# Kernel optimization log

Measured on AMD Instinct MI355X. Metric: run time of the kernel, lower is better.

The kernel has to match this reference:

```python
import jax, jax.numpy as jnp
import numpy as np

B, T, N, KH, DH, KS = 8, 64, 128, 8, 64, 3  # batch, num_step, num_vertex, heads, head_dim, kernel
D = KH * DH
EPS = 1e-5


def setup_inputs() -> dict:
    key = jax.random.key(0)
    ks = jax.random.split(key, 8)
    s = 0.02
    return {
        "X": jax.random.normal(ks[0], (B, T, N, D), dtype=jnp.float32),
        # causal conv Q/K: torch Conv2d weight [out, in, 1, ks]
        "Wq": jax.random.normal(ks[1], (D, D, 1, KS), dtype=jnp.float32) * s,
        "bq": jnp.zeros((D,), jnp.float32),
        "gq": jnp.ones((D,), jnp.float32),
        "betaq": jnp.zeros((D,), jnp.float32),
        "mq": jnp.zeros((D,), jnp.float32),
        "vq": jnp.ones((D,), jnp.float32),
        "Wk": jax.random.normal(ks[2], (D, D, 1, KS), dtype=jnp.float32) * s,
        "bk": jnp.zeros((D,), jnp.float32),
        "gk": jnp.ones((D,), jnp.float32),
        "betak": jnp.zeros((D,), jnp.float32),
        "mk": jnp.zeros((D,), jnp.float32),
        "vk": jnp.ones((D,), jnp.float32),
        # torch Linear weights [out, in]
        "Wv": jax.random.normal(ks[3], (D, D), dtype=jnp.float32) * s,
        "bv": jnp.zeros((D,), jnp.float32),
        "Wo": jax.random.normal(ks[4], (D, D), dtype=jnp.float32) * s,
        "bo": jnp.zeros((D,), jnp.float32),
    }


def _causal_conv(x, W, b):
    # x: [B, D, N, T]; left-pad time by ks-1 == torch pad-both-then-slice[:-pad]
    pad = W.shape[-1] - 1
    y = jax.lax.conv_general_dilated(
        x, W, window_strides=(1, 1), padding=((0, 0), (pad, 0)),
        dimension_numbers=("NCHW", "OIHW", "NCHW"))
    return y + b[None, :, None, None]


def _bn(x, g, beta, m, v):
    # eval-mode BatchNorm2d over channel dim 1
    inv = jax.lax.rsqrt(v + EPS)
    return (x - m[None, :, None, None]) * (g * inv)[None, :, None, None] + beta[None, :, None, None]


def reference(X, Wq, bq, gq, betaq, mq, vq, Wk, bk, gk, betak, mk, vk, Wv, bv, Wo, bo):
    b, t, n, dm = X.shape
    X_ = X.transpose(0, 3, 2, 1)                       # [B, D, N, T]
    q = _bn(_causal_conv(X_, Wq, bq), gq, betaq, mq, vq).transpose(0, 3, 2, 1)  # [B,T,N,D]
    k = _bn(_causal_conv(X_, Wk, bk), gk, betak, mk, vk).transpose(0, 3, 2, 1)  # [B,T,N,D]
    v = jnp.einsum("btnd,ed->btne", X, Wv) + bv        # FC_v
    # split heads (equivalent to split/cat along batch in the original)
    qh = q.reshape(b, t, n, KH, DH)
    kh = k.reshape(b, t, n, KH, DH)
    vh = v.reshape(b, t, n, KH, DH)
    scores = jnp.einsum("bqnhd,bpnhd->bnhqp", qh, kh) * (DH ** -0.5)  # [B,N,H,T,T]
    attn = jax.nn.softmax(scores, axis=-1)
    out = jnp.einsum("bnhqp,bpnhd->bqnhd", attn, vh).reshape(b, t, n, dm)
    out = jnp.einsum("btnd,ed->btne", out, Wo) + bo    # FC
    return out  # [B, T, N, D]
```

## Files before the change

kernel.cpp:

```cpp
#include <hip/hip_runtime.h>

typedef unsigned short u16;
typedef u16    u16x4  __attribute__((ext_vector_type(4)));
typedef u16    u16x8  __attribute__((ext_vector_type(8)));
typedef __bf16 bf16x8 __attribute__((ext_vector_type(8)));
typedef float  f32x4  __attribute__((ext_vector_type(4)));
typedef float  f32x16 __attribute__((ext_vector_type(16)));

#define DEV static __device__ __forceinline__

DEV float bf2f(u16 h) {
    union { unsigned int u; float f; } c; c.u = ((unsigned int)h) << 16; return c.f;
}
DEV u16 f2bf(float f) {
    union { float f; unsigned int u; } c; c.f = f;
    unsigned int u = c.u + 0x7FFFu + ((c.u >> 16) & 1u);
    return (u16)(u >> 16);
}
DEV bf16x8 ld8(const u16* p) {
    return __builtin_bit_cast(bf16x8, *(const u16x8*)p);
}
DEV void gload_lds16(const u16* g, u16* l) {
    __builtin_amdgcn_global_load_lds((__attribute__((address_space(1))) void*)g,
                                     (__attribute__((address_space(3))) void*)l,
                                     16, 0, 0);
}

__global__ __launch_bounds__(256) void f32_to_bf16(
    const float* __restrict__ src, u16* __restrict__ dst, int n)
{
    int i = (blockIdx.x * 256 + threadIdx.x) * 4;
    if (i < n) {
        f32x4 v = *(const f32x4*)(src + i);
        u16x4 o;
        o[0] = f2bf(v[0]); o[1] = f2bf(v[1]); o[2] = f2bf(v[2]); o[3] = f2bf(v[3]);
        *(u16x4*)(dst + i) = o;
    }
}

__global__ __launch_bounds__(256) void prep_weights(
    const float* __restrict__ Wq, const float* __restrict__ gq, const float* __restrict__ vq,
    const float* __restrict__ Wk, const float* __restrict__ gk, const float* __restrict__ vk,
    u16* __restrict__ Wqt, u16* __restrict__ Wkt)
{
    int idx = blockIdx.x * 256 + threadIdx.x;
    int mat = idx >= 786432;
    int rem = idx - mat * 786432;
    int tap = rem / 262144;
    int oi  = rem - tap * 262144;
    int o = oi >> 9, i = oi & 511;
    const float* W = mat ? Wk : Wq;
    const float* g = mat ? gk : gq;
    const float* v = mat ? vk : vq;
    float s = g[o] * rsqrtf(v[o] + 1e-5f) * (mat ? 1.0f : 0.125f);
    float w = W[(o * 512 + i) * 3 + tap] * s;
    (mat ? Wkt : Wqt)[(tap * 512 + o) * 512 + i] = f2bf(w);
}

__global__ __launch_bounds__(256) void prep_bias(
    const float* bq, const float* gq, const float* betaq, const float* mq, const float* vq,
    const float* bk, const float* gk, const float* betak, const float* mk, const float* vk,
    float* __restrict__ biasq, float* __restrict__ biask)
{
    int o = blockIdx.x * 256 + threadIdx.x;
    if (o < 512) {
        float sq = gq[o] * rsqrtf(vq[o] + 1e-5f);
        biasq[o] = ((bq[o] - mq[o]) * sq + betaq[o]) * 0.125f;
        float sk = gk[o] * rsqrtf(vk[o] + 1e-5f);
        biask[o] = (bk[o] - mk[o]) * sk + betak[o];
    }
}

__global__ __launch_bounds__(256) void qkv_gemm(
    const u16* __restrict__ Xb,
    const u16* __restrict__ Wqt, const u16* __restrict__ Wkt, const u16* __restrict__ Wv,
    const float* __restrict__ biasq, const float* __restrict__ biask, const float* __restrict__ bv,
    u16* __restrict__ Qa, u16* __restrict__ Ka, u16* __restrict__ Va, int b0)
{
    __shared__ __align__(16) u16 As[128 * 64];
    __shared__ __align__(16) u16 Bs[128 * 64];

    const int which = blockIdx.x >> 2;
    const int cb    = (blockIdx.x & 3) * 128;
    const int rt    = blockIdx.y;
    const int brel  = rt >> 6;
    const int b     = b0 + brel;
    const int t     = rt & 63;

    const int tid  = threadIdx.x;
    const int wave = tid >> 6;
    const int lane = tid & 63;
    const int wm   = (wave & 1) * 64;
    const int wn   = (wave >> 1) * 64;
    const int l31  = lane & 31;
    const int q5   = lane >> 5;

    f32x16 acc[2][2];
#pragma unroll
    for (int mi = 0; mi < 2; mi++)
#pragma unroll
        for (int ni = 0; ni < 2; ni++)
#pragma unroll
            for (int e = 0; e < 16; e++) acc[mi][ni][e] = 0.f;

    const int ntaps = (which == 2) ? 1 : 3;
    const u16* Wbase0 = (which == 0) ? Wqt : (which == 1) ? Wkt : Wv;

    for (int tap = 0; tap < ntaps; ++tap) {
        int tsrc = (which == 2) ? t : (t + tap - 2);
        if (tsrc < 0) continue;
        const u16* Abase = Xb + ((size_t)(b * 64 + tsrc) * 128) * 512;
        const u16* Wbase = Wbase0 + (which == 2 ? 0 : (size_t)tap * 262144);

        for (int kk = 0; kk < 512; kk += 64) {
            __syncthreads();
#pragma unroll
            for (int i = 0; i < 4; ++i) {
                int p   = i * 256 + tid;
                int row = p >> 3;
                int sl  = (p & 7) ^ (row & 7);
                gload_lds16(Abase + (size_t)row * 512 + kk + sl * 8, As + p * 8);
                gload_lds16(Wbase + (size_t)(cb + row) * 512 + kk + sl * 8, Bs + p * 8);
            }
            __syncthreads();

#pragma unroll
            for (int half = 0; half < 2; ++half) {
                bf16x8 af[2][2], bf[2][2];
#pragma unroll
                for (int mi = 0; mi < 2; mi++) {
                    int r = wm + mi * 32 + l31;
#pragma unroll
                    for (int j = 0; j < 2; j++) {
                        int k2 = half * 2 + j;
                        af[mi][j] = ld8(As + ((r * 64 + k2 * 16 + q5 * 8) ^ ((r & 7) << 3)));
                    }
                }
#pragma unroll
                for (int ni = 0; ni < 2; ni++) {
                    int c = wn + ni * 32 + l31;
#pragma unroll
                    for (int j = 0; j < 2; j++) {
                        int k2 = half * 2 + j;
                        bf[ni][j] = ld8(Bs + ((c * 64 + k2 * 16 + q5 * 8) ^ ((c & 7) << 3)));
                    }
                }
#pragma unroll
                for (int j = 0; j < 2; j++)
#pragma unroll
                    for (int mi = 0; mi < 2; mi++)
#pragma unroll
                        for (int ni = 0; ni < 2; ni++)
                            acc[mi][ni] = __builtin_amdgcn_mfma_f32_32x32x16_bf16(
                                af[mi][j], bf[ni][j], acc[mi][ni], 0, 0, 0);
            }
        }
    }

    float biasv[2];
#pragma unroll
    for (int ni = 0; ni < 2; ni++) {
        int c = cb + wn + ni * 32 + l31;
        biasv[ni] = (which == 0) ? biasq[c] : (which == 1) ? biask[c] : bv[c];
    }
    u16* Outp = (which == 0) ? Qa : (which == 1) ? Ka : Va;
#pragma unroll
    for (int mi = 0; mi < 2; mi++) {
#pragma unroll
        for (int ni = 0; ni < 2; ni++) {
            int c = cb + wn + ni * 32 + l31;
            int h = c >> 6, dd = c & 63;
#pragma unroll
            for (int r = 0; r < 16; r++) {
                int n = wm + mi * 32 + (r & 3) + ((r >> 2) << 3) + (q5 << 2);
                float val = acc[mi][ni][r] + biasv[ni];
                size_t idx = ((((size_t)(brel * 128 + n)) * 8 + h) * 64 + t) * 64 + dd;
                Outp[idx] = f2bf(val);
            }
        }
    }
}

__global__ __launch_bounds__(256) void attn_kernel(
    const u16* __restrict__ Qa, const u16* __restrict__ Ka, const u16* __restrict__ Va,
    u16* __restrict__ AO)
{
    __shared__ __align__(16) u16 Qs[64 * 72];
    __shared__ __align__(16) u16 Ks[64 * 72];
    __shared__ __align__(16) u16 Vt[64 * 72];
    __shared__ __align__(16) u16 Ps[64 * 72];

    const int h = blockIdx.x, n = blockIdx.y, brel = blockIdx.z;
    const int tid = threadIdx.x, wave = tid >> 6, lane = tid & 63;
    const int l15 = lane & 15, q4 = lane >> 4;
    const size_t base = ((size_t)((brel * 128 + n) * 8 + h)) * 4096;

#pragma unroll
    for (int i = 0; i < 2; i++) {
        int chunk = i * 256 + tid;
        int row = chunk >> 3, kc = chunk & 7;
        u16x8 vq = *(const u16x8*)(Qa + base + chunk * 8);
        u16x8 vk = *(const u16x8*)(Ka + base + chunk * 8);
        u16x8 vv = *(const u16x8*)(Va + base + chunk * 8);
        *(u16x8*)(Qs + row * 72 + kc * 8) = vq;
        *(u16x8*)(Ks + row * 72 + kc * 8) = vk;
#pragma unroll
        for (int j = 0; j < 8; j++) Vt[(kc * 8 + j) * 72 + row] = vv[j];
    }
    __syncthreads();

    f32x4 s[4];
#pragma unroll
    for (int ni = 0; ni < 4; ni++) s[ni] = f32x4{0.f, 0.f, 0.f, 0.f};
    bf16x8 aq[2];
#pragma unroll
    for (int ks = 0; ks < 2; ks++)
        aq[ks] = ld8(Qs + (wave * 16 + l15) * 72 + ks * 32 + q4 * 8);
#pragma unroll
    for (int ni = 0; ni < 4; ni++) {
        int p = ni * 16 + l15;
#pragma unroll
        for (int ks = 0; ks < 2; ks++) {
            bf16x8 bk8 = ld8(Ks + p * 72 + ks * 32 + q4 * 8);
            s[ni] = __builtin_amdgcn_mfma_f32_16x16x32_bf16(aq[ks], bk8, s[ni], 0, 0, 0);
        }
    }

    float rmax[4], rsum[4], inv[4];
#pragma unroll
    for (int r = 0; r < 4; r++)
        rmax[r] = fmaxf(fmaxf(s[0][r], s[1][r]), fmaxf(s[2][r], s[3][r]));
#pragma unroll
    for (int m = 1; m < 16; m <<= 1)
#pragma unroll
        for (int r = 0; r < 4; r++)
            rmax[r] = fmaxf(rmax[r], __shfl_xor(rmax[r], m, 64));
    float e[4][4];
#pragma unroll
    for (int r = 0; r < 4; r++) rsum[r] = 0.f;
#pragma unroll
    for (int ni = 0; ni < 4; ni++)
#pragma unroll
        for (int r = 0; r < 4; r++) {
            e[ni][r] = __expf(s[ni][r] - rmax[r]);
            rsum[r] += e[ni][r];
        }
#pragma unroll
    for (int m = 1; m < 16; m <<= 1)
#pragma unroll
        for (int r = 0; r < 4; r++)
            rsum[r] += __shfl_xor(rsum[r], m, 64);
#pragma unroll
    for (int r = 0; r < 4; r++) inv[r] = 1.0f / rsum[r];

#pragma unroll
    for (int ni = 0; ni < 4; ni++)
#pragma unroll
        for (int r = 0; r < 4; r++)
            Ps[(wave * 16 + q4 * 4 + r) * 72 + ni * 16 + l15] = f2bf(e[ni][r]);
    __syncthreads();

    f32x4 o[4];
#pragma unroll
    for (int ni = 0; ni < 4; ni++) o[ni] = f32x4{0.f, 0.f, 0.f, 0.f};
    bf16x8 ap[2];
#pragma unroll
    for (int ks = 0; ks < 2; ks++)
        ap[ks] = ld8(Ps + (wave * 16 + l15) * 72 + ks * 32 + q4 * 8);
#pragma unroll
    for (int ni = 0; ni < 4; ni++) {
        int dd = ni * 16 + l15;
#pragma unroll
        for (int ks = 0; ks < 2; ks++) {
            bf16x8 bv8 = ld8(Vt + dd * 72 + ks * 32 + q4 * 8);
            o[ni] = __builtin_amdgcn_mfma_f32_16x16x32_bf16(ap[ks], bv8, o[ni], 0, 0, 0);
        }
    }

#pragma unroll
    for (int ni = 0; ni < 4; ni++) {
        int dd = ni * 16 + l15;
#pragma unroll
        for (int r = 0; r < 4; r++) {
            int tt = wave * 16 + q4 * 4 + r;
            AO[base + tt * 64 + dd] = f2bf(o[ni][r] * inv[r]);
        }
    }
}

__global__ __launch_bounds__(256) void proj_gemm(
    const u16* __restrict__ AO, const u16* __restrict__ Wo, const float* __restrict__ bo,
    float* __restrict__ Out, int b0)
{
    __shared__ __align__(16) u16 As[128 * 64];
    __shared__ __align__(16) u16 Bs[128 * 64];

    const int cb   = blockIdx.x * 128;
    const int rt   = blockIdx.y;
    const int brel = rt >> 6;
    const int b    = b0 + brel;
    const int t    = rt & 63;

    const int tid  = threadIdx.x;
    const int wave = tid >> 6;
    const int lane = tid & 63;
    const int wm   = (wave & 1) * 64;
    const int wn   = (wave >> 1) * 64;
    const int l31  = lane & 31;
    const int q5   = lane >> 5;

    f32x16 acc[2][2];
#pragma unroll
    for (int mi = 0; mi < 2; mi++)
#pragma unroll
        for (int ni = 0; ni < 2; ni++)
#pragma unroll
            for (int e = 0; e < 16; e++) acc[mi][ni][e] = 0.f;

    for (int kk = 0; kk < 512; kk += 64) {
        __syncthreads();
#pragma unroll
        for (int i = 0; i < 4; ++i) {
            int p   = i * 256 + tid;
            int row = p >> 3;
            int sl  = (p & 7) ^ (row & 7);
            int k   = kk + sl * 8;
            int hh  = k >> 6, d0 = k & 63;
            const u16* ga = AO + ((((size_t)(brel * 128 + row)) * 8 + hh) * 64 + t) * 64 + d0;
            gload_lds16(ga, As + p * 8);
            gload_lds16(Wo + (size_t)(cb + row) * 512 + k, Bs + p * 8);
        }
        __syncthreads();

#pragma unroll
        for (int half = 0; half < 2; ++half) {
            bf16x8 af[2][2], bf[2][2];
#pragma unroll
            for (int mi = 0; mi < 2; mi++) {
                int r = wm + mi * 32 + l31;
#pragma unroll
                for (int j = 0; j < 2; j++) {
                    int k2 = half * 2 + j;
                    af[mi][j] = ld8(As + ((r * 64 + k2 * 16 + q5 * 8) ^ ((r & 7) << 3)));
                }
            }
#pragma unroll
            for (int ni = 0; ni < 2; ni++) {
                int c = wn + ni * 32 + l31;
#pragma unroll
                for (int j = 0; j < 2; j++) {
                    int k2 = half * 2 + j;
                    bf[ni][j] = ld8(Bs + ((c * 64 + k2 * 16 + q5 * 8) ^ ((c & 7) << 3)));
                }
            }
#pragma unroll
            for (int j = 0; j < 2; j++)
#pragma unroll
                for (int mi = 0; mi < 2; mi++)
#pragma unroll
                    for (int ni = 0; ni < 2; ni++)
                        acc[mi][ni] = __builtin_amdgcn_mfma_f32_32x32x16_bf16(
                            af[mi][j], bf[ni][j], acc[mi][ni], 0, 0, 0);
        }
    }

#pragma unroll
    for (int mi = 0; mi < 2; mi++) {
#pragma unroll
        for (int ni = 0; ni < 2; ni++) {
            int c = cb + wn + ni * 32 + l31;
            float bias = bo[c];
#pragma unroll
            for (int r = 0; r < 16; r++) {
                int n = wm + mi * 32 + (r & 3) + ((r >> 2) << 3) + (q5 << 2);
                float val = acc[mi][ni][r] + bias;
                size_t idx = (((size_t)(b * 64 + t)) * 128 + n) * 512 + c;
                Out[idx] = val;
            }
        }
    }
}

extern "C" void kernel_launch(void* const* d_in, const int* in_sizes, int n_in,
                              void* d_out, int out_size, void* d_ws, size_t ws_size,
                              hipStream_t stream)
{
    const float* X     = (const float*)d_in[0];
    const float* Wq    = (const float*)d_in[1];
    const float* bq    = (const float*)d_in[2];
    const float* gq    = (const float*)d_in[3];
    const float* betaq = (const float*)d_in[4];
    const float* mq    = (const float*)d_in[5];
    const float* vq    = (const float*)d_in[6];
    const float* Wk    = (const float*)d_in[7];
    const float* bk    = (const float*)d_in[8];
    const float* gk    = (const float*)d_in[9];
    const float* betak = (const float*)d_in[10];
    const float* mk    = (const float*)d_in[11];
    const float* vk    = (const float*)d_in[12];
    const float* Wv    = (const float*)d_in[13];
    const float* bv    = (const float*)d_in[14];
    const float* Wo    = (const float*)d_in[15];
    const float* bo    = (const float*)d_in[16];
    float* outp = (float*)d_out;
    u16*   ws   = (u16*)d_ws;

    const size_t XTOT   = 33554432;
    const size_t XSLICE = 4194304;

    const bool big = ws_size >= (size_t)206000000;

    u16 *Xb, *Qa, *Ka, *Wqt;
    if (big) {
        Xb  = ws;
        Qa  = ws + XTOT;
        Ka  = Qa + XTOT;
        Wqt = Ka + XTOT;
    } else {
        Xb  = ws;
        Qa  = ws + XSLICE;
        Ka  = Qa + XSLICE;
        Wqt = Ka + XSLICE;
    }
    u16* Wkt = Wqt + 786432;
    u16* Wvb = Wkt + 786432;
    u16* Wob = Wvb + 262144;
    float* biasq = (float*)(Wob + 262144);
    float* biask = biasq + 512;

    hipLaunchKernelGGL(prep_weights, dim3(6144), dim3(256), 0, stream,
                       Wq, gq, vq, Wk, gk, vk, Wqt, Wkt);
    hipLaunchKernelGGL(prep_bias, dim3(2), dim3(256), 0, stream,
                       bq, gq, betaq, mq, vq, bk, gk, betak, mk, vk, biasq, biask);
    hipLaunchKernelGGL(f32_to_bf16, dim3(256), dim3(256), 0, stream, Wv, Wvb, 262144);
    hipLaunchKernelGGL(f32_to_bf16, dim3(256), dim3(256), 0, stream, Wo, Wob, 262144);

    if (big) {
        u16* Va = (u16*)d_out;
        hipLaunchKernelGGL(f32_to_bf16, dim3(32768), dim3(256), 0, stream,
                           X, Xb, (int)XTOT);
        hipLaunchKernelGGL(qkv_gemm, dim3(12, 512), dim3(256), 0, stream,
                           Xb, Wqt, Wkt, Wvb, biasq, biask, bv, Qa, Ka, Va, 0);
        hipLaunchKernelGGL(attn_kernel, dim3(8, 128, 8), dim3(256), 0, stream,
                           Qa, Ka, Va, Qa);
        hipLaunchKernelGGL(proj_gemm, dim3(4, 512), dim3(256), 0, stream,
                           Qa, Wob, bo, outp, 0);
    } else {
        for (int p = 0; p < 8; ++p) {
            u16* Va = (u16*)d_out + (size_t)p * 2 * XSLICE;
            hipLaunchKernelGGL(f32_to_bf16, dim3(4096), dim3(256), 0, stream,
                               X + (size_t)p * XSLICE, Xb, (int)XSLICE);
            hipLaunchKernelGGL(qkv_gemm, dim3(12, 64), dim3(256), 0, stream,
                               Xb - (size_t)p * XSLICE, Wqt, Wkt, Wvb,
                               biasq, biask, bv, Qa, Ka, Va, p);
            hipLaunchKernelGGL(attn_kernel, dim3(8, 128, 1), dim3(256), 0, stream,
                               Qa, Ka, Va, Qa);
            hipLaunchKernelGGL(proj_gemm, dim3(4, 64), dim3(256), 0, stream,
                               Qa, Wob, bo, outp, p);
        }
    }
}
```

Before: 634.1 us.

## Replace QKV GEMM with 256x256-tile double-buffered 8-wave kernel

Rewrites the fused Q/K/V projection as a 512-thread kernel. Each block computes a 256-row (two timesteps) by 256-column tile. The conv taps are folded into a single K=1536 loop using a tap-interleaved weight layout, and padded timesteps load from a zero buffer instead of taking a branch. LDS is double-buffered, with prefetch interleaved between MFMA phases, s_setprio, and block-index remapping for XCD locality. This is meant to cut LDS/global traffic per FLOP and hide load latency, at the cost of high register pressure (occupancy 1) and more barriers.

```diff
diff --git a/kernel.cpp b/kernel.cpp
--- a/kernel.cpp
+++ b/kernel.cpp
@@ -5,7 +5,6 @@
 typedef u16    u16x8  __attribute__((ext_vector_type(8)));
 typedef __bf16 bf16x8 __attribute__((ext_vector_type(8)));
 typedef float  f32x4  __attribute__((ext_vector_type(4)));
-typedef float  f32x16 __attribute__((ext_vector_type(16)));
 
 #define DEV static __device__ __forceinline__
 
@@ -25,6 +24,12 @@
                                      (__attribute__((address_space(3))) void*)l,
                                      16, 0, 0);
 }
+DEV void bar() {
+    asm volatile("" ::: "memory");
+    __builtin_amdgcn_s_barrier();
+    asm volatile("" ::: "memory");
+}
+#define VMCNT(n) asm volatile("s_waitcnt vmcnt(" #n ")" ::: "memory")
 
 __global__ __launch_bounds__(256) void f32_to_bf16(
     const float* __restrict__ src, u16* __restrict__ dst, int n)
@@ -54,13 +59,13 @@
     const float* v = mat ? vk : vq;
     float s = g[o] * rsqrtf(v[o] + 1e-5f) * (mat ? 1.0f : 0.125f);
     float w = W[(o * 512 + i) * 3 + tap] * s;
-    (mat ? Wkt : Wqt)[(tap * 512 + o) * 512 + i] = f2bf(w);
+    (mat ? Wkt : Wqt)[(o * 3 + tap) * 512 + i] = f2bf(w);
 }
 
 __global__ __launch_bounds__(256) void prep_bias(
     const float* bq, const float* gq, const float* betaq, const float* mq, const float* vq,
     const float* bk, const float* gk, const float* betak, const float* mk, const float* vk,
-    float* __restrict__ biasq, float* __restrict__ biask)
+    float* __restrict__ biasq, float* __restrict__ biask, u16* __restrict__ zb)
 {
     int o = blockIdx.x * 256 + threadIdx.x;
     if (o < 512) {
@@ -69,113 +74,166 @@
         float sk = gk[o] * rsqrtf(vk[o] + 1e-5f);
         biask[o] = (bk[o] - mk[o]) * sk + betak[o];
     }
-}
-
-__global__ __launch_bounds__(256) void qkv_gemm(
+    if (blockIdx.x == 0 && threadIdx.x < 64) zb[threadIdx.x] = 0;
+}
+
+__global__ __launch_bounds__(512, 1) void qkv8(
     const u16* __restrict__ Xb,
-    const u16* __restrict__ Wqt, const u16* __restrict__ Wkt, const u16* __restrict__ Wv,
+    const u16* __restrict__ Wq3, const u16* __restrict__ Wk3, const u16* __restrict__ Wv1,
     const float* __restrict__ biasq, const float* __restrict__ biask, const float* __restrict__ bv,
+    const u16* __restrict__ zbuf,
     u16* __restrict__ Qa, u16* __restrict__ Ka, u16* __restrict__ Va, int b0)
 {
-    __shared__ __align__(16) u16 As[128 * 64];
-    __shared__ __align__(16) u16 Bs[128 * 64];
-
-    const int which = blockIdx.x >> 2;
-    const int cb    = (blockIdx.x & 3) * 128;
-    const int rt    = blockIdx.y;
-    const int brel  = rt >> 6;
+    __shared__ __align__(16) u16 As[2 * 16384];
+    __shared__ __align__(16) u16 Bs[2 * 16384];
+
+    const int total = gridDim.x;
+    const int cpx   = total >> 3;
+    const int s     = blockIdx.x;
+    const int w     = (s & 7) * cpx + (s >> 3);
+    const int wc    = w % 6;
+    const int bt    = w / 6;
+    const int which = wc >> 1;
+    const int cb    = (wc & 1) * 256;
+    const int tpair = bt & 31;
+    const int brel  = bt >> 5;
     const int b     = b0 + brel;
-    const int t     = rt & 63;
 
     const int tid  = threadIdx.x;
     const int wave = tid >> 6;
     const int lane = tid & 63;
-    const int wm   = (wave & 1) * 64;
-    const int wn   = (wave >> 1) * 64;
-    const int l31  = lane & 31;
-    const int q5   = lane >> 5;
-
-    f32x16 acc[2][2];
-#pragma unroll
-    for (int mi = 0; mi < 2; mi++)
-#pragma unroll
-        for (int ni = 0; ni < 2; ni++)
-#pragma unroll
-            for (int e = 0; e < 16; e++) acc[mi][ni][e] = 0.f;
-
-    const int ntaps = (which == 2) ? 1 : 3;
-    const u16* Wbase0 = (which == 0) ? Wqt : (which == 1) ? Wkt : Wv;
-
-    for (int tap = 0; tap < ntaps; ++tap) {
-        int tsrc = (which == 2) ? t : (t + tap - 2);
-        if (tsrc < 0) continue;
-        const u16* Abase = Xb + ((size_t)(b * 64 + tsrc) * 128) * 512;
-        const u16* Wbase = Wbase0 + (which == 2 ? 0 : (size_t)tap * 262144);
-
-        for (int kk = 0; kk < 512; kk += 64) {
-            __syncthreads();
-#pragma unroll
-            for (int i = 0; i < 4; ++i) {
-                int p   = i * 256 + tid;
-                int row = p >> 3;
-                int sl  = (p & 7) ^ (row & 7);
-                gload_lds16(Abase + (size_t)row * 512 + kk + sl * 8, As + p * 8);
-                gload_lds16(Wbase + (size_t)(cb + row) * 512 + kk + sl * 8, Bs + p * 8);
-            }
-            __syncthreads();
-
-#pragma unroll
-            for (int half = 0; half < 2; ++half) {
-                bf16x8 af[2][2], bf[2][2];
-#pragma unroll
-                for (int mi = 0; mi < 2; mi++) {
-                    int r = wm + mi * 32 + l31;
-#pragma unroll
-                    for (int j = 0; j < 2; j++) {
-                        int k2 = half * 2 + j;
-                        af[mi][j] = ld8(As + ((r * 64 + k2 * 16 + q5 * 8) ^ ((r & 7) << 3)));
-                    }
-                }
-#pragma unroll
-                for (int ni = 0; ni < 2; ni++) {
-                    int c = wn + ni * 32 + l31;
-#pragma unroll
-                    for (int j = 0; j < 2; j++) {
-                        int k2 = half * 2 + j;
-                        bf[ni][j] = ld8(Bs + ((c * 64 + k2 * 16 + q5 * 8) ^ ((c & 7) << 3)));
-                    }
-                }
-#pragma unroll
-                for (int j = 0; j < 2; j++)
-#pragma unroll
-                    for (int mi = 0; mi < 2; mi++)
-#pragma unroll
-                        for (int ni = 0; ni < 2; ni++)
-                            acc[mi][ni] = __builtin_amdgcn_mfma_f32_32x32x16_bf16(
-                                af[mi][j], bf[ni][j], acc[mi][ni], 0, 0, 0);
-            }
-        }
-    }
-
-    float biasv[2];
-#pragma unroll
-    for (int ni = 0; ni < 2; ni++) {
-        int c = cb + wn + ni * 32 + l31;
-        biasv[ni] = (which == 0) ? biasq[c] : (which == 1) ? biask[c] : bv[c];
-    }
+    const int l15  = lane & 15;
+    const int q4   = lane >> 4;
+    const int wn   = wave;
+
+    const u16* WB = (which == 0) ? Wq3 : (which == 1) ? Wk3 : Wv1;
+    const int  KW = (which == 2) ? 512 : 1536;
+    const int  NT = (which == 2) ? 8 : 24;
+
+    f32x4 acc[16][2];
+#pragma unroll
+    for (int a = 0; a < 16; ++a)
+#pragma unroll
+        for (int ni = 0; ni < 2; ++ni) acc[a][ni] = f32x4{0.f, 0.f, 0.f, 0.f};
+
+    auto stageA = [&](int kt, int bufp, int h) {
+        int tap  = (which == 2) ? 0 : (kt >> 3);
+        int kb   = (which == 2) ? (kt << 6) : ((kt & 7) << 6);
+        int tsrc = 2 * tpair + h + ((which == 2) ? 0 : (tap - 2));
+#pragma unroll
+        for (int j = 0; j < 2; ++j) {
+            int slot = h * 1024 + j * 512 + tid;
+            int r = slot >> 3, sl = slot & 7;
+            const u16* src = (tsrc < 0) ? zbuf
+                : Xb + ((size_t)((b * 64 + tsrc) * 128 + (r & 127))) * 512 + kb
+                     + ((sl ^ (r & 7)) << 3);
+            gload_lds16(src, As + bufp * 16384 + slot * 8);
+        }
+    };
+    auto stageB = [&](int kt, int bufp, int h) {
+#pragma unroll
+        for (int j = 0; j < 2; ++j) {
+            int slot = h * 1024 + j * 512 + tid;
+            int r = slot >> 3, sl = slot & 7;
+            const u16* src = WB + (size_t)(cb + r) * KW + (kt << 6)
+                           + ((sl ^ (r & 7)) << 3);
+            gload_lds16(src, Bs + bufp * 16384 + slot * 8);
+        }
+    };
+
+#define PHASE_READ_B() \
+    _Pragma("unroll") \
+    for (int ni = 0; ni < 2; ++ni) { \
+        _Pragma("unroll") \
+        for (int ks = 0; ks < 2; ++ks) { \
+            int rr = wn * 32 + ni * 16 + l15; \
+            bfr[ni][ks] = ld8(Bcur + ((rr * 64 + ks * 32 + q4 * 8) ^ ((l15 & 7) << 3))); \
+        } \
+    }
+
+#define PHASE_READ_A(q) \
+    _Pragma("unroll") \
+    for (int mi = 0; mi < 4; ++mi) { \
+        _Pragma("unroll") \
+        for (int ks = 0; ks < 2; ++ks) { \
+            int rr = (q) * 64 + mi * 16 + l15; \
+            af[mi][ks] = ld8(Acur + ((rr * 64 + ks * 32 + q4 * 8) ^ ((l15 & 7) << 3))); \
+        } \
+    }
+
+#define PHASE_MFMA(q) \
+    __builtin_amdgcn_s_setprio(1); \
+    _Pragma("unroll") \
+    for (int ks = 0; ks < 2; ++ks) \
+        _Pragma("unroll") \
+        for (int mi = 0; mi < 4; ++mi) \
+            _Pragma("unroll") \
+            for (int ni = 0; ni < 2; ++ni) \
+                acc[(q) * 4 + mi][ni] = __builtin_amdgcn_mfma_f32_16x16x32_bf16( \
+                    af[mi][ks], bfr[ni][ks], acc[(q) * 4 + mi][ni], 0, 0, 0); \
+    __builtin_amdgcn_s_setprio(0);
+
+    stageB(0, 0, 0); stageB(0, 0, 1);
+    stageA(0, 0, 0); stageA(0, 0, 1);
+    VMCNT(2);
+    bar();
+
+    for (int kt = 0; kt < NT; ++kt) {
+        const int cur = kt & 1, nxt = cur ^ 1;
+        const bool pf = (kt + 1 < NT);
+        const u16* Acur = As + cur * 16384;
+        const u16* Bcur = Bs + cur * 16384;
+        bf16x8 af[4][2], bfr[2][2];
+
+        PHASE_READ_B();
+        PHASE_READ_A(0);
+        if (pf) stageB(kt + 1, nxt, 0);
+        bar();
+        PHASE_MFMA(0);
+        bar();
+
+        PHASE_READ_A(1);
+        if (pf) stageB(kt + 1, nxt, 1);
+        bar();
+        PHASE_MFMA(1);
+        VMCNT(4);
+        bar();
+
+        PHASE_READ_A(2);
+        if (pf) stageA(kt + 1, nxt, 0);
+        bar();
+        PHASE_MFMA(2);
+        bar();
+
+        PHASE_READ_A(3);
+        if (pf) stageA(kt + 1, nxt, 1);
+        bar();
+        PHASE_MFMA(3);
+        VMCNT(2);
+        bar();
+    }
+
+#undef PHASE_READ_B
+#undef PHASE_READ_A
+#undef PHASE_MFMA
+
+    const float* biasp = (which == 0) ? biasq : (which == 1) ? biask : bv;
+    float bias2[2];
+#pragma unroll
+    for (int ni = 0; ni < 2; ++ni) bias2[ni] = biasp[cb + wn * 32 + ni * 16 + l15];
     u16* Outp = (which == 0) ? Qa : (which == 1) ? Ka : Va;
 #pragma unroll
-    for (int mi = 0; mi < 2; mi++) {
-#pragma unroll
-        for (int ni = 0; ni < 2; ni++) {
-            int c = cb + wn + ni * 32 + l31;
+    for (int a = 0; a < 16; ++a) {
+#pragma unroll
+        for (int ni = 0; ni < 2; ++ni) {
+            int c = cb + wn * 32 + ni * 16 + l15;
             int h = c >> 6, dd = c & 63;
 #pragma unroll
-            for (int r = 0; r < 16; r++) {
-                int n = wm + mi * 32 + (r & 3) + ((r >> 2) << 3) + (q5 << 2);
-                float val = acc[mi][ni][r] + biasv[ni];
-                size_t idx = ((((size_t)(brel * 128 + n)) * 8 + h) * 64 + t) * 64 + dd;
-                Outp[idx] = f2bf(val);
+            for (int r = 0; r < 4; ++r) {
+                int row = a * 16 + q4 * 4 + r;
+                int n = row & 127, tt = 2 * tpair + (row >> 7);
+                float val = acc[a][ni][r] + bias2[ni];
+                Outp[((((size_t)(brel * 128 + n)) * 8 + h) * 64 + tt) * 64 + dd] = f2bf(val);
             }
         }
     }
@@ -309,7 +367,8 @@
     const int l31  = lane & 31;
     const int q5   = lane >> 5;
 
-    f32x16 acc[2][2];
+    typedef float f32x16_t __attribute__((ext_vector_type(16)));
+    f32x16_t acc[2][2];
 #pragma unroll
     for (int mi = 0; mi < 2; mi++)
 #pragma unroll
@@ -427,11 +486,12 @@
     u16* Wob = Wvb + 262144;
     float* biasq = (float*)(Wob + 262144);
     float* biask = biasq + 512;
+    u16*   zbuf  = (u16*)(biask + 512);
 
     hipLaunchKernelGGL(prep_weights, dim3(6144), dim3(256), 0, stream,
                        Wq, gq, vq, Wk, gk, vk, Wqt, Wkt);
     hipLaunchKernelGGL(prep_bias, dim3(2), dim3(256), 0, stream,
-                       bq, gq, betaq, mq, vq, bk, gk, betak, mk, vk, biasq, biask);
+                       bq, gq, betaq, mq, vq, bk, gk, betak, mk, vk, biasq, biask, zbuf);
     hipLaunchKernelGGL(f32_to_bf16, dim3(256), dim3(256), 0, stream, Wv, Wvb, 262144);
     hipLaunchKernelGGL(f32_to_bf16, dim3(256), dim3(256), 0, stream, Wo, Wob, 262144);
 
@@ -439,8 +499,8 @@
         u16* Va = (u16*)d_out;
         hipLaunchKernelGGL(f32_to_bf16, dim3(32768), dim3(256), 0, stream,
                            X, Xb, (int)XTOT);
-        hipLaunchKernelGGL(qkv_gemm, dim3(12, 512), dim3(256), 0, stream,
-                           Xb, Wqt, Wkt, Wvb, biasq, biask, bv, Qa, Ka, Va, 0);
+        hipLaunchKernelGGL(qkv8, dim3(1536), dim3(512), 0, stream,
+                           Xb, Wqt, Wkt, Wvb, biasq, biask, bv, zbuf, Qa, Ka, Va, 0);
         hipLaunchKernelGGL(attn_kernel, dim3(8, 128, 8), dim3(256), 0, stream,
                            Qa, Ka, Va, Qa);
         hipLaunchKernelGGL(proj_gemm, dim3(4, 512), dim3(256), 0, stream,
@@ -450,9 +510,9 @@
             u16* Va = (u16*)d_out + (size_t)p * 2 * XSLICE;
             hipLaunchKernelGGL(f32_to_bf16, dim3(4096), dim3(256), 0, stream,
                                X + (size_t)p * XSLICE, Xb, (int)XSLICE);
-            hipLaunchKernelGGL(qkv_gemm, dim3(12, 64), dim3(256), 0, stream,
+            hipLaunchKernelGGL(qkv8, dim3(192), dim3(512), 0, stream,
                                Xb - (size_t)p * XSLICE, Wqt, Wkt, Wvb,
-                               biasq, biask, bv, Qa, Ka, Va, p);
+                               biasq, biask, bv, zbuf, Qa, Ka, Va, p);
             hipLaunchKernelGGL(attn_kernel, dim3(8, 128, 1), dim3(256), 0, stream,
                                Qa, Ka, Va, Qa);
             hipLaunchKernelGGL(proj_gemm, dim3(4, 64), dim3(256), 0, stream,
```

Result: faster. 614.3 us (-3.1%).

## Restructure QKV GEMM with flattened tap-K loop, 16x16 MFMA, XCD block swizzle

Applied to the files above, without the earlier changes.

Q/K conv weights are stored tap-interleaved per output channel, so the causal conv becomes one contiguous K=1536 GEMM loop. Out-of-range taps now load from a zero buffer instead of being skipped. The QKV kernel moves from 32x32x16 to 16x16x32 MFMA tiles and adds a launch-bounds occupancy hint of 4. Both GEMMs remap block IDs across XCDs so neighbouring tiles share L2. The trade-off is extra MFMA work on zeroed taps for the first time steps, plus a small new workspace region.

```diff
diff --git a/kernel.cpp b/kernel.cpp
--- a/kernel.cpp
+++ b/kernel.cpp
@@ -5,7 +5,6 @@
 typedef u16    u16x8  __attribute__((ext_vector_type(8)));
 typedef __bf16 bf16x8 __attribute__((ext_vector_type(8)));
 typedef float  f32x4  __attribute__((ext_vector_type(4)));
-typedef float  f32x16 __attribute__((ext_vector_type(16)));
 
 #define DEV static __device__ __forceinline__
 
@@ -54,13 +53,13 @@
     const float* v = mat ? vk : vq;
     float s = g[o] * rsqrtf(v[o] + 1e-5f) * (mat ? 1.0f : 0.125f);
     float w = W[(o * 512 + i) * 3 + tap] * s;
-    (mat ? Wkt : Wqt)[(tap * 512 + o) * 512 + i] = f2bf(w);
+    (mat ? Wkt : Wqt)[(o * 3 + tap) * 512 + i] = f2bf(w);
 }
 
 __global__ __launch_bounds__(256) void prep_bias(
     const float* bq, const float* gq, const float* betaq, const float* mq, const float* vq,
     const float* bk, const float* gk, const float* betak, const float* mk, const float* vk,
-    float* __restrict__ biasq, float* __restrict__ biask)
+    float* __restrict__ biasq, float* __restrict__ biask, u16* __restrict__ zb)
 {
     int o = blockIdx.x * 256 + threadIdx.x;
     if (o < 512) {
@@ -69,111 +68,108 @@
         float sk = gk[o] * rsqrtf(vk[o] + 1e-5f);
         biask[o] = (bk[o] - mk[o]) * sk + betak[o];
     }
-}
-
-__global__ __launch_bounds__(256) void qkv_gemm(
+    if (blockIdx.x == 0 && threadIdx.x < 64) zb[threadIdx.x] = 0;
+}
+
+__global__ __launch_bounds__(256, 4) void qkv_gemm(
     const u16* __restrict__ Xb,
-    const u16* __restrict__ Wqt, const u16* __restrict__ Wkt, const u16* __restrict__ Wv,
+    const u16* __restrict__ Wq3, const u16* __restrict__ Wk3, const u16* __restrict__ Wv1,
     const float* __restrict__ biasq, const float* __restrict__ biask, const float* __restrict__ bv,
+    const u16* __restrict__ zbuf,
     u16* __restrict__ Qa, u16* __restrict__ Ka, u16* __restrict__ Va, int b0)
 {
     __shared__ __align__(16) u16 As[128 * 64];
     __shared__ __align__(16) u16 Bs[128 * 64];
 
-    const int which = blockIdx.x >> 2;
-    const int cb    = (blockIdx.x & 3) * 128;
-    const int rt    = blockIdx.y;
-    const int brel  = rt >> 6;
+    const int total = gridDim.y * 12;
+    const int hid   = blockIdx.y * 12 + blockIdx.x;
+    const int w     = (hid & 7) * (total >> 3) + (hid >> 3);
+    const int col   = w % 12;
+    const int bt    = w / 12;
+    const int which = col >> 2;
+    const int cb    = (col & 3) * 128;
+    const int t     = bt & 63;
+    const int brel  = bt >> 6;
     const int b     = b0 + brel;
-    const int t     = rt & 63;
 
     const int tid  = threadIdx.x;
     const int wave = tid >> 6;
     const int lane = tid & 63;
     const int wm   = (wave & 1) * 64;
     const int wn   = (wave >> 1) * 64;
-    const int l31  = lane & 31;
-    const int q5   = lane >> 5;
-
-    f32x16 acc[2][2];
-#pragma unroll
-    for (int mi = 0; mi < 2; mi++)
-#pragma unroll
-        for (int ni = 0; ni < 2; ni++)
-#pragma unroll
-            for (int e = 0; e < 16; e++) acc[mi][ni][e] = 0.f;
-
-    const int ntaps = (which == 2) ? 1 : 3;
-    const u16* Wbase0 = (which == 0) ? Wqt : (which == 1) ? Wkt : Wv;
-
-    for (int tap = 0; tap < ntaps; ++tap) {
-        int tsrc = (which == 2) ? t : (t + tap - 2);
-        if (tsrc < 0) continue;
-        const u16* Abase = Xb + ((size_t)(b * 64 + tsrc) * 128) * 512;
-        const u16* Wbase = Wbase0 + (which == 2 ? 0 : (size_t)tap * 262144);
-
-        for (int kk = 0; kk < 512; kk += 64) {
-            __syncthreads();
-#pragma unroll
-            for (int i = 0; i < 4; ++i) {
-                int p   = i * 256 + tid;
-                int row = p >> 3;
-                int sl  = (p & 7) ^ (row & 7);
-                gload_lds16(Abase + (size_t)row * 512 + kk + sl * 8, As + p * 8);
-                gload_lds16(Wbase + (size_t)(cb + row) * 512 + kk + sl * 8, Bs + p * 8);
-            }
-            __syncthreads();
-
-#pragma unroll
-            for (int half = 0; half < 2; ++half) {
-                bf16x8 af[2][2], bf[2][2];
-#pragma unroll
-                for (int mi = 0; mi < 2; mi++) {
-                    int r = wm + mi * 32 + l31;
-#pragma unroll
-                    for (int j = 0; j < 2; j++) {
-                        int k2 = half * 2 + j;
-                        af[mi][j] = ld8(As + ((r * 64 + k2 * 16 + q5 * 8) ^ ((r & 7) << 3)));
-                    }
-                }
-#pragma unroll
-                for (int ni = 0; ni < 2; ni++) {
-                    int c = wn + ni * 32 + l31;
-#pragma unroll
-                    for (int j = 0; j < 2; j++) {
-                        int k2 = half * 2 + j;
-                        bf[ni][j] = ld8(Bs + ((c * 64 + k2 * 16 + q5 * 8) ^ ((c & 7) << 3)));
-                    }
-                }
-#pragma unroll
-                for (int j = 0; j < 2; j++)
-#pragma unroll
-                    for (int mi = 0; mi < 2; mi++)
-#pragma unroll
-                        for (int ni = 0; ni < 2; ni++)
-                            acc[mi][ni] = __builtin_amdgcn_mfma_f32_32x32x16_bf16(
-                                af[mi][j], bf[ni][j], acc[mi][ni], 0, 0, 0);
-            }
-        }
-    }
-
-    float biasv[2];
-#pragma unroll
-    for (int ni = 0; ni < 2; ni++) {
-        int c = cb + wn + ni * 32 + l31;
-        biasv[ni] = (which == 0) ? biasq[c] : (which == 1) ? biask[c] : bv[c];
+    const int l15  = lane & 15;
+    const int q4   = lane >> 4;
+
+    f32x4 acc[4][4];
+#pragma unroll
+    for (int i = 0; i < 4; i++)
+#pragma unroll
+        for (int j = 0; j < 4; j++) acc[i][j] = f32x4{0.f, 0.f, 0.f, 0.f};
+
+    const u16* WB = (which == 0) ? Wq3 : (which == 1) ? Wk3 : Wv1;
+    const int  KW = (which == 2) ? 512 : 1536;
+    const int  NT = (which == 2) ? 8 : 24;
+
+    for (int kt = 0; kt < NT; ++kt) {
+        const int kwo = kt << 6;
+        const int tap = kwo >> 9;
+        const int ko  = kwo & 511;
+        const int tsrc = (which == 2) ? t : (t + tap - 2);
+        const u16* Abase = (tsrc < 0) ? nullptr
+            : Xb + ((size_t)((b * 64 + tsrc) * 128)) * 512 + ko;
+
+        __syncthreads();
+#pragma unroll
+        for (int i = 0; i < 4; ++i) {
+            int c   = i * 256 + tid;
+            int row = c >> 3;
+            int sl  = c & 7;
+            int ss  = sl ^ (row & 7);
+            const u16* sa = Abase ? Abase + (size_t)row * 512 + ss * 8 : zbuf;
+            gload_lds16(sa, As + c * 8);
+            gload_lds16(WB + (size_t)(cb + row) * KW + kwo + ss * 8, Bs + c * 8);
+        }
+        __syncthreads();
+
+#pragma unroll
+        for (int ks = 0; ks < 2; ++ks) {
+            bf16x8 af[4], bf[4];
+#pragma unroll
+            for (int mi = 0; mi < 4; mi++) {
+                int r = wm + mi * 16 + l15;
+                af[mi] = ld8(As + ((r * 64 + ks * 32 + q4 * 8) ^ ((r & 7) << 3)));
+            }
+#pragma unroll
+            for (int ni = 0; ni < 4; ni++) {
+                int cc = wn + ni * 16 + l15;
+                bf[ni] = ld8(Bs + ((cc * 64 + ks * 32 + q4 * 8) ^ ((cc & 7) << 3)));
+            }
+#pragma unroll
+            for (int mi = 0; mi < 4; mi++)
+#pragma unroll
+                for (int ni = 0; ni < 4; ni++)
+                    acc[mi][ni] = __builtin_amdgcn_mfma_f32_16x16x32_bf16(
+                        af[mi], bf[ni], acc[mi][ni], 0, 0, 0);
+        }
+    }
+
+    float bias[4];
+#pragma unroll
+    for (int ni = 0; ni < 4; ni++) {
+        int c = cb + wn + ni * 16 + l15;
+        bias[ni] = (which == 0) ? biasq[c] : (which == 1) ? biask[c] : bv[c];
     }
     u16* Outp = (which == 0) ? Qa : (which == 1) ? Ka : Va;
 #pragma unroll
-    for (int mi = 0; mi < 2; mi++) {
-#pragma unroll
-        for (int ni = 0; ni < 2; ni++) {
-            int c = cb + wn + ni * 32 + l31;
+    for (int mi = 0; mi < 4; mi++) {
+#pragma unroll
+        for (int ni = 0; ni < 4; ni++) {
+            int c = cb + wn + ni * 16 + l15;
             int h = c >> 6, dd = c & 63;
 #pragma unroll
-            for (int r = 0; r < 16; r++) {
-                int n = wm + mi * 32 + (r & 3) + ((r >> 2) << 3) + (q5 << 2);
-                float val = acc[mi][ni][r] + biasv[ni];
+            for (int r = 0; r < 4; r++) {
+                int n = wm + mi * 16 + q4 * 4 + r;
+                float val = acc[mi][ni][r] + bias[ni];
                 size_t idx = ((((size_t)(brel * 128 + n)) * 8 + h) * 64 + t) * 64 + dd;
                 Outp[idx] = f2bf(val);
             }
@@ -295,11 +291,14 @@
     __shared__ __align__(16) u16 As[128 * 64];
     __shared__ __align__(16) u16 Bs[128 * 64];
 
-    const int cb   = blockIdx.x * 128;
-    const int rt   = blockIdx.y;
-    const int brel = rt >> 6;
-    const int b    = b0 + brel;
-    const int t    = rt & 63;
+    const int total = gridDim.y * 4;
+    const int hid   = blockIdx.y * 4 + blockIdx.x;
+    const int w     = (hid & 7) * (total >> 3) + (hid >> 3);
+    const int cb    = (w & 3) * 128;
+    const int rt    = w >> 2;
+    const int brel  = rt >> 6;
+    const int b     = b0 + brel;
+    const int t     = rt & 63;
 
     const int tid  = threadIdx.x;
     const int wave = tid >> 6;
@@ -309,7 +308,8 @@
     const int l31  = lane & 31;
     const int q5   = lane >> 5;
 
-    f32x16 acc[2][2];
+    typedef float f32x16_t __attribute__((ext_vector_type(16)));
+    f32x16_t acc[2][2];
 #pragma unroll
     for (int mi = 0; mi < 2; mi++)
 #pragma unroll
@@ -427,11 +427,12 @@
     u16* Wob = Wvb + 262144;
     float* biasq = (float*)(Wob + 262144);
     float* biask = biasq + 512;
+    u16*   zbuf  = (u16*)(biask + 512);
 
     hipLaunchKernelGGL(prep_weights, dim3(6144), dim3(256), 0, stream,
                        Wq, gq, vq, Wk, gk, vk, Wqt, Wkt);
     hipLaunchKernelGGL(prep_bias, dim3(2), dim3(256), 0, stream,
-                       bq, gq, betaq, mq, vq, bk, gk, betak, mk, vk, biasq, biask);
+                       bq, gq, betaq, mq, vq, bk, gk, betak, mk, vk, biasq, biask, zbuf);
     hipLaunchKernelGGL(f32_to_bf16, dim3(256), dim3(256), 0, stream, Wv, Wvb, 262144);
     hipLaunchKernelGGL(f32_to_bf16, dim3(256), dim3(256), 0, stream, Wo, Wob, 262144);
 
@@ -440,7 +441,7 @@
         hipLaunchKernelGGL(f32_to_bf16, dim3(32768), dim3(256), 0, stream,
                            X, Xb, (int)XTOT);
         hipLaunchKernelGGL(qkv_gemm, dim3(12, 512), dim3(256), 0, stream,
-                           Xb, Wqt, Wkt, Wvb, biasq, biask, bv, Qa, Ka, Va, 0);
+                           Xb, Wqt, Wkt, Wvb, biasq, biask, bv, zbuf, Qa, Ka, Va, 0);
         hipLaunchKernelGGL(attn_kernel, dim3(8, 128, 8), dim3(256), 0, stream,
                            Qa, Ka, Va, Qa);
         hipLaunchKernelGGL(proj_gemm, dim3(4, 512), dim3(256), 0, stream,
@@ -452,7 +453,7 @@
                                X + (size_t)p * XSLICE, Xb, (int)XSLICE);
             hipLaunchKernelGGL(qkv_gemm, dim3(12, 64), dim3(256), 0, stream,
                                Xb - (size_t)p * XSLICE, Wqt, Wkt, Wvb,
-                               biasq, biask, bv, Qa, Ka, Va, p);
+                               biasq, biask, bv, zbuf, Qa, Ka, Va, p);
             hipLaunchKernelGGL(attn_kernel, dim3(8, 128, 1), dim3(256), 0, stream,
                                Qa, Ka, Va, Qa);
             hipLaunchKernelGGL(proj_gemm, dim3(4, 64), dim3(256), 0, stream,
```

After: 631.7 us. Within noise of the previous version (-0.4%).
